# Kernel optimization log

Hardware: AMD Instinct MI355X
Metric: run time of the kernel (lower is better)

Reference implementation:

```python
import jax, jax.numpy as jnp
import numpy as np

IN_C = 256
OUT_C = 256
KS = 3
PAD = 1
EPS = 1e-5
BLOCK_SIZE = 256  # largest power of 2 dividing IN_C
NUM_BLOCKS = IN_C // BLOCK_SIZE


def golay_sequence(n):
    pow2 = 1
    while pow2 < n:
        pow2 *= 2
    a = np.array([1.0], dtype=np.float32)
    b = np.array([1.0], dtype=np.float32)
    while len(a) < pow2:
        a, b = np.concatenate([a, b]), np.concatenate([a, -b])
    return a[:n]


def fwht(x):
    """Unnormalized fast Walsh-Hadamard transform over the last axis (Sylvester order)."""
    base = x.shape[:-1]
    n = x.shape[-1]
    h = 1
    while h < n:
        y = x.reshape(base + (n // (2 * h), 2, h))
        a, c = y[..., 0, :], y[..., 1, :]
        x = jnp.stack([a + c, a - c], axis=-2).reshape(base + (n,))
        h *= 2
    return x


def setup_inputs() -> dict:
    key = jax.random.key(0)
    k1, k2, k3 = jax.random.split(key, 3)
    x = jax.random.normal(k1, (32, IN_C, 56, 56), dtype=jnp.float32)
    fan_in = IN_C * KS * KS
    W = jax.random.normal(k2, (OUT_C, IN_C, KS, KS), dtype=jnp.float32) / np.sqrt(fan_in)
    b = jax.random.normal(k3, (OUT_C,), dtype=jnp.float32) * 0.01
    rms_w = jnp.ones((IN_C,), dtype=jnp.float32)
    return {"x": x, "W": W, "b": b, "rms_w": rms_w}


def reference(x, W, b, rms_w):
    n, c, h, w = x.shape
    golay = jnp.asarray(golay_sequence(c)).reshape(1, c, 1, 1)
    x = x * golay                                    # Golay elementwise multiply
    x = jnp.transpose(x, (0, 2, 3, 1))               # NCHW -> NHWC
    x = x.reshape(n, h, w, NUM_BLOCKS, BLOCK_SIZE)
    x = fwht(x)                                      # blockwise Hadamard butterfly
    x = x.reshape(n, h, w, c)
    # RMSNorm over channel dim
    x = x * jax.lax.rsqrt(jnp.mean(x * x, axis=-1, keepdims=True) + EPS) * rms_w
    x = jnp.transpose(x, (0, 3, 1, 2))               # NHWC -> NCHW
    out = jax.lax.conv_general_dilated(
        x, W, window_strides=(1, 1), padding=((PAD, PAD), (PAD, PAD)),
        dimension_numbers=("NCHW", "OIHW", "NCHW"))
    return out + b[None, :, None, None]
```

## Files before the change

kernel.cpp:

```cpp
#include <hip/hip_runtime.h>
#include <hip/hip_bf16.h>

typedef short v8s __attribute__((ext_vector_type(8)));
typedef float v4f __attribute__((ext_vector_type(4)));
typedef float v16f __attribute__((ext_vector_type(16)));
typedef unsigned short u16;

#define PROW 58
#define PCOL 64

static constexpr size_t A_CC_STRIDE = (size_t)32 * PROW * PCOL * 32;
static constexpr size_t A_BYTES     = 8 * A_CC_STRIDE * 2;
static constexpr size_t WB_ELEMS    = (size_t)9 * 8 * 256 * 32;

__device__ __forceinline__ void gl2lds16(const void* gptr, void* lptr) {
  auto g = (const __attribute__((address_space(1))) unsigned int*)gptr;
  auto l = (__attribute__((address_space(3))) unsigned int*)lptr;
  __builtin_amdgcn_global_load_lds(g, l, 16, 0, 0);
}

__device__ __forceinline__ u16 f2bf(float f) {
  __hip_bfloat16 h = __float2bfloat16(f);
  union { __hip_bfloat16 b; u16 u; } cv; cv.b = h; return cv.u;
}

struct HgTab {
  u16 v[16 * 8 * 64 * 8];
  constexpr HgTab() : v{} {
    for (int ks = 0; ks < 16; ks++)
      for (int nt = 0; nt < 8; nt++)
        for (int l = 0; l < 64; l++)
          for (int j = 0; j < 8; j++) {
            int c  = ks * 16 + ((l >> 5) << 3) + j;
            int cp = (nt << 5) + (l & 31);
            int s  = (__builtin_popcount((unsigned)(c & cp)) +
                      __builtin_popcount((unsigned)(c & (c >> 1)))) & 1;
            v[(((ks << 3) + nt) << 9) + (l << 3) + j] = (u16)(s ? 0xBF80 : 0x3F80);
          }
  }
};
static_assert(sizeof(HgTab) == 131072, "HgTab size");
__device__ const HgTab HG{};

__global__ __launch_bounds__(256, 4) void fwht_kernel(
    const float* __restrict__ x, const float* __restrict__ rms_w,
    u16* __restrict__ A)
{
  __shared__ float ssbuf[2][64];

  const int tid = threadIdx.x;
  const int y = blockIdx.x;
  const int n = blockIdx.y;

  const int lane = tid & 63;
  const int wv   = tid >> 6;
  const int mt   = wv & 1;
  const int nh   = wv >> 1;
  const int l31  = lane & 31;
  const int h    = lane >> 5;

  const int pos  = mt * 32 + l31;
  const int posl = pos > 55 ? 55 : pos;
  const float* src = x + (size_t)n * 802816 + (size_t)y * 56 + posl;

  v16f acc[4];
  #pragma unroll
  for (int nt = 0; nt < 4; nt++)
    #pragma unroll
    for (int e = 0; e < 16; e++)
      acc[nt][e] = 0.0f;

  #pragma unroll 4
  for (int ks = 0; ks < 16; ks++) {
    const float* sc0 = src + (size_t)(ks * 16 + h * 8) * 3136;
    v8s ah, al;
    #pragma unroll
    for (int j = 0; j < 8; j++) {
      float v = sc0[(size_t)j * 3136];
      unsigned u  = __float_as_uint(v);
      unsigned hu = u & 0xFFFF0000u;
      float r = v - __uint_as_float(hu);
      ah[j] = (short)(hu >> 16);
      al[j] = (short)f2bf(r);
    }
    #pragma unroll
    for (int nt = 0; nt < 4; nt++) {
      v8s b = *(const v8s*)(HG.v + ((size_t)(((ks * 8) + nh * 4 + nt) * 64 + lane)) * 8);
      acc[nt] = __builtin_amdgcn_mfma_f32_32x32x16_bf16(ah, b, acc[nt], 0, 0, 0);
      acc[nt] = __builtin_amdgcn_mfma_f32_32x32x16_bf16(al, b, acc[nt], 0, 0, 0);
    }
  }

  #pragma unroll
  for (int g = 0; g < 16; g++) {
    float s = acc[0][g] * acc[0][g] + acc[1][g] * acc[1][g]
            + acc[2][g] * acc[2][g] + acc[3][g] * acc[3][g];
    #pragma unroll
    for (int m = 1; m <= 16; m <<= 1) s += __shfl_xor(s, m, 64);
    if (l31 == 0)
      ssbuf[nh][mt * 32 + (g & 3) + 8 * (g >> 2) + 4 * h] = s;
  }
  __syncthreads();

  float rwv[4];
  #pragma unroll
  for (int nt = 0; nt < 4; nt++)
    rwv[nt] = rms_w[nh * 128 + nt * 32 + l31];

  const int jj  = lane & 7;
  const int icq = l31 >> 3;

  #pragma unroll
  for (int g = 0; g < 16; g++) {
    const int rg   = (g & 3) + 8 * (g >> 2) + 4 * h;
    const int posg = mt * 32 + rg;
    float ssum = ssbuf[0][posg] + ssbuf[1][posg];
    float sc = rsqrtf(ssum * (1.0f / 256.0f) + 1e-5f);
    if (posg < 56) {
      const int col = posg + 1;
      const int sw  = (col >> 1) & 3;
      const int qs  = ((icq ^ sw) << 3) | jj;
      const size_t rowoff = (size_t)col * 32 + qs;
      #pragma unroll
      for (int nt = 0; nt < 4; nt++) {
        const int cc = nh * 4 + nt;
        size_t go = (((size_t)cc * 32 + n) * PROW + (y + 1)) * 2048 + rowoff;
        A[go] = f2bf(acc[nt][g] * sc * rwv[nt]);
      }
    }
  }

  {
    const v8s z = {0,0,0,0,0,0,0,0};
    int cc = tid >> 5, s = tid & 31;
    size_t rb = (((size_t)cc * 32 + n) * PROW + (y + 1)) * 2048;
    if (s < 4) *(v8s*)(A + rb + s * 8) = z;
    else       *(v8s*)(A + rb + 57 * 32 + (s - 4) * 8) = z;
  }
  if (y == 0 || y == 55) {
    const v8s z = {0,0,0,0,0,0,0,0};
    const int r = (y == 0) ? 0 : 57;
    #pragma unroll
    for (int i = 0; i < 8; i++) {
      int c = tid + 256 * i;
      int cc = c >> 8, rem = c & 255;
      size_t go = (((size_t)cc * 32 + n) * PROW + r) * 2048 + rem * 8;
      *(v8s*)(A + go) = z;
    }
  }
}

__global__ __launch_bounds__(256) void wconv_kernel(
    const float* __restrict__ Wf, u16* __restrict__ Wb)
{
  int t = blockIdx.x * 256 + threadIdx.x;
  int j = t & 7;
  int icq_st = (t >> 3) & 3;
  int oc = (t >> 5) & 255;
  int cc = (t >> 13) & 7;
  int kk = t >> 16;
  int icq = icq_st ^ ((oc >> 1) & 3);
  int ic = cc * 32 + icq * 8 + j;
  int ky = kk / 3, kx = kk - ky * 3;
  float w = Wf[((oc * 256 + ic) * 3 + ky) * 3 + kx];
  Wb[t] = f2bf(w);
}

__global__ __launch_bounds__(256, 4) void conv_kernel(
    const u16* __restrict__ A, const u16* __restrict__ Wb,
    const float* __restrict__ bias, float* __restrict__ out)
{
  __shared__ __align__(16) u16 As[4 * PCOL * 32];
  __shared__ __align__(16) u16 Bs[3 * 128 * 32];

  const int tid  = threadIdx.x;
  const int lane = tid & 63;
  const int wv   = tid >> 6;
  const int wm   = wv & 1;
  const int wn   = wv >> 1;
  const int m31  = lane & 31;
  const int kh8  = lane >> 5;

  const int ocb = blockIdx.x;
  const int y0  = blockIdx.y * 2;
  const int n   = blockIdx.z;

  const u16* gA = A + ((size_t)n * PROW + y0) * 2048;

  v16f acc[2][2];
  #pragma unroll
  for (int i = 0; i < 2; i++)
    #pragma unroll
    for (int j = 0; j < 2; j++)
      #pragma unroll
      for (int e = 0; e < 16; e++)
        acc[i][j][e] = 0.0f;

  int ub[2][2];
  #pragma unroll
  for (int nf = 0; nf < 2; nf++)
    #pragma unroll
    for (int kh = 0; kh < 2; kh++) {
      int ocl = wn * 64 + nf * 32 + m31;
      int q = kh * 2 + kh8;
      ub[nf][kh] = (ocl * 4 + (q ^ ((ocl >> 1) & 3))) * 8;
    }

  auto stageA = [&](int cc) {
    const u16* g = gA + (size_t)cc * A_CC_STRIDE + tid * 8;
    u16* d = As + tid * 8;
    #pragma unroll
    for (int k = 0; k < 4; k++)
      gl2lds16(g + k * 2048, d + k * 2048);
  };
  auto stageB = [&](int cc, int ky) {
    #pragma unroll
    for (int kx = 0; kx < 3; kx++) {
      const int kk = ky * 3 + kx;
      const u16* g = Wb + ((kk * 8 + cc) * 8192 + ocb * 4096) + tid * 8;
      u16* d = Bs + kx * 4096 + tid * 8;
      gl2lds16(g, d);
      gl2lds16(g + 2048, d + 2048);
    }
  };

  for (int cc = 0; cc < 8; cc++) {
    __syncthreads();
    stageA(cc);
    stageB(cc, 0);
    __syncthreads();
    #pragma unroll
    for (int ky = 0; ky < 3; ky++) {
      #pragma unroll
      for (int kx = 0; kx < 3; kx++) {
        v8s af[2][2];
        #pragma unroll
        for (int mf = 0; mf < 2; mf++)
          #pragma unroll
          for (int kh = 0; kh < 2; kh++) {
            int col = mf * 32 + m31 + kx;
            col = col > 63 ? 63 : col;
            int q = kh * 2 + kh8;
            int ua = (((wm + ky) * PCOL + col) * 4 + (q ^ ((col >> 1) & 3))) * 8;
            af[mf][kh] = *(const v8s*)(As + ua);
          }
        v8s bf[2][2];
        const u16* bsb = Bs + kx * 4096;
        #pragma unroll
        for (int nf = 0; nf < 2; nf++)
          #pragma unroll
          for (int kh = 0; kh < 2; kh++)
            bf[nf][kh] = *(const v8s*)(bsb + ub[nf][kh]);
        #pragma unroll
        for (int mf = 0; mf < 2; mf++)
          #pragma unroll
          for (int nf = 0; nf < 2; nf++) {
            acc[mf][nf] = __builtin_amdgcn_mfma_f32_32x32x16_bf16(af[mf][0], bf[nf][0], acc[mf][nf], 0, 0, 0);
            acc[mf][nf] = __builtin_amdgcn_mfma_f32_32x32x16_bf16(af[mf][1], bf[nf][1], acc[mf][nf], 0, 0, 0);
          }
      }
      if (ky < 2) {
        __syncthreads();
        stageB(cc, ky + 1);
        __syncthreads();
      }
    }
  }

  const int yrow = y0 + wm;
  #pragma unroll
  for (int nf = 0; nf < 2; nf++) {
    const int oc = ocb * 128 + wn * 64 + nf * 32 + m31;
    const float bb = bias[oc];
    float* orow = out + ((size_t)(n * 256 + oc) * 56 + yrow) * 56;
    #pragma unroll
    for (int mf = 0; mf < 2; mf++) {
      #pragma unroll
      for (int g = 0; g < 4; g++) {
        const int x0 = mf * 32 + 8 * g + 4 * kh8;
        if (x0 < 56) {
          v4f val = { acc[mf][nf][4*g+0] + bb, acc[mf][nf][4*g+1] + bb,
                      acc[mf][nf][4*g+2] + bb, acc[mf][nf][4*g+3] + bb };
          *(v4f*)(orow + x0) = val;
        }
      }
    }
  }
}

extern "C" void kernel_launch(void* const* d_in, const int* in_sizes, int n_in,
                              void* d_out, int out_size, void* d_ws, size_t ws_size,
                              hipStream_t stream)
{
  const float* x     = (const float*)d_in[0];
  const float* Wf    = (const float*)d_in[1];
  const float* bias  = (const float*)d_in[2];
  const float* rms_w = (const float*)d_in[3];
  float* out = (float*)d_out;

  if (ws_size < A_BYTES + WB_ELEMS * 2) return;

  u16* Abf = (u16*)d_ws;
  u16* Wb  = (u16*)((char*)d_ws + A_BYTES);

  fwht_kernel<<<dim3(56, 32), 256, 0, stream>>>(x, rms_w, Abf);
  wconv_kernel<<<dim3((int)(WB_ELEMS / 256)), 256, 0, stream>>>(Wf, Wb);
  conv_kernel<<<dim3(2, 28, 32), 256, 0, stream>>>(Abf, Wb, bias, out);
}
```

Baseline: 396.9 us.

## Double-buffer FWHT input tiles in LDS via async global-to-LDS loads

The FWHT kernel no longer reads x with strided per-lane global loads inside the MFMA loop. Each wave now copies its 16x64 channel-by-position tile into a private LDS double buffer using 16-byte global_load_lds. The load for step ks+1 is issued before step ks is computed, with explicit vmcnt waits and scheduling barriers, and the Hadamard-table fragments are fetched at the top of each step. The aim is to hide global memory latency behind MFMA work, at the cost of 32 KB of extra LDS per block, which may reduce occupancy, and of fragile hand-written wait counts.

```diff
diff --git a/kernel.cpp b/kernel.cpp
--- a/kernel.cpp
+++ b/kernel.cpp
@@ -24,7 +24,7 @@
   union { __hip_bfloat16 b; u16 u; } cv; cv.b = h; return cv.u;
 }
 
-struct HgTab {
+struct alignas(16) HgTab {
   u16 v[16 * 8 * 64 * 8];
   constexpr HgTab() : v{} {
     for (int ks = 0; ks < 16; ks++)
@@ -46,6 +46,7 @@
     const float* __restrict__ x, const float* __restrict__ rms_w,
     u16* __restrict__ A)
 {
+  __shared__ __align__(16) float xs[4][2][16][64];
   __shared__ float ssbuf[2][64];
 
   const int tid = threadIdx.x;
@@ -61,7 +62,20 @@
 
   const int pos  = mt * 32 + l31;
   const int posl = pos > 55 ? 55 : pos;
-  const float* src = x + (size_t)n * 802816 + (size_t)y * 56 + posl;
+
+  const float* xrow = x + (size_t)n * 802816 + (size_t)y * 56;
+  const int rr = lane >> 4;
+  int c4 = (lane & 15) * 4; if (c4 > 52) c4 = 52;
+
+  float* db0 = &xs[wv][0][0][0];
+  float* db1 = &xs[wv][1][0][0];
+
+  auto stage = [&](int ks, float* db) {
+    const float* sb = xrow + (size_t)(ks * 16 + rr) * 3136 + c4;
+    #pragma unroll
+    for (int k = 0; k < 4; k++)
+      gl2lds16(sb + (size_t)(k * 4) * 3136, db + k * 256 + lane * 4);
+  };
 
   v16f acc[4];
   #pragma unroll
@@ -70,13 +84,29 @@
     for (int e = 0; e < 16; e++)
       acc[nt][e] = 0.0f;
 
-  #pragma unroll 4
+  stage(0, db0);
+
+  #pragma unroll
   for (int ks = 0; ks < 16; ks++) {
-    const float* sc0 = src + (size_t)(ks * 16 + h * 8) * 3136;
+    float* cb = (ks & 1) ? db1 : db0;
+    float* nb = (ks & 1) ? db0 : db1;
+
+    v8s bfr[4];
+    #pragma unroll
+    for (int nt = 0; nt < 4; nt++)
+      bfr[nt] = *(const v8s*)(HG.v + ((size_t)(((ks * 8) + nh * 4 + nt) * 64 + lane)) * 8);
+    __builtin_amdgcn_sched_barrier(0);
+
+    if (ks < 15) stage(ks + 1, nb);
+    __builtin_amdgcn_sched_barrier(0);
+
+    asm volatile("s_waitcnt vmcnt(4)" ::: "memory");
+    __builtin_amdgcn_sched_barrier(0);
+
     v8s ah, al;
     #pragma unroll
     for (int j = 0; j < 8; j++) {
-      float v = sc0[(size_t)j * 3136];
+      float v = cb[(h * 8 + j) * 64 + posl];
       unsigned u  = __float_as_uint(v);
       unsigned hu = u & 0xFFFF0000u;
       float r = v - __uint_as_float(hu);
@@ -85,9 +115,8 @@
     }
     #pragma unroll
     for (int nt = 0; nt < 4; nt++) {
-      v8s b = *(const v8s*)(HG.v + ((size_t)(((ks * 8) + nh * 4 + nt) * 64 + lane)) * 8);
-      acc[nt] = __builtin_amdgcn_mfma_f32_32x32x16_bf16(ah, b, acc[nt], 0, 0, 0);
-      acc[nt] = __builtin_amdgcn_mfma_f32_32x32x16_bf16(al, b, acc[nt], 0, 0, 0);
+      acc[nt] = __builtin_amdgcn_mfma_f32_32x32x16_bf16(ah, bfr[nt], acc[nt], 0, 0, 0);
+      acc[nt] = __builtin_amdgcn_mfma_f32_32x32x16_bf16(al, bfr[nt], acc[nt], 0, 0, 0);
     }
   }
 
```

New measurement: 347.4 us. 1.14x faster.
